# Kernel optimization log

Measured on AMD Instinct MI355X. Metric: run time of the kernel, lower is better.

## Reference

```python
import jax, jax.numpy as jnp
import numpy as np

STRIDE, PAD, DIL = 1, 1, 1
EPS = 1e-12
RHO_LIM = 1.0 - 1e-6
PI = jnp.pi


def clamp_pg(x, lo=0.0):
    # clamp value but pass gradient through (clamp_preserve_grad)
    return x + jax.lax.stop_gradient(jnp.maximum(x, lo) - x)


def setup_inputs() -> dict:
    key = jax.random.key(0)
    B, N, T, K = 8, 128, 1024, 3
    k = jax.random.uniform(key, (B, B, N, T, 2), dtype=jnp.float32)
    leak = jnp.array(1.0, dtype=jnp.float32)
    alpha = jnp.full((1, 1, K), 1.0 / K, dtype=jnp.float32)
    beta = jnp.array(0.0, dtype=jnp.float32)
    return {"k": k, "leak": leak, "alpha": alpha, "beta": beta}


def reference(k, leak, alpha, beta):
    k_gp, k_ntk = k[..., 0], k[..., 1]          # (B,B,N,T) each
    B, _, N, T = k_gp.shape

    # v[b,t] = k_gp[b,b,0,t]  (diagonal over batch dims, first lag)
    ar = jnp.arange(B)
    v = k_gp[ar, ar, 0, :]                      # (B,T)
    v_pad = jnp.pad(v, ((0, 0), (0, N - 1)))    # (B, T+N-1)

    v_xx = v[:, None, None, :]                  # (B,1,1,T)
    idx = jnp.arange(N)[:, None] + jnp.arange(T)[None, :]  # (N,T)
    v_yy = v_pad[:, idx][None]                  # (1,B,N,T): v_pad[b, n+t]

    # calculate_statistics
    std_x = jnp.sqrt(jnp.maximum(v_xx, 0.0))
    std_y = jnp.sqrt(jnp.maximum(v_yy, 0.0))
    denom = jnp.maximum(std_x * std_y, EPS)
    rho = jnp.clip(k_gp / denom, -RHO_LIM, RHO_LIM)  # (B,B,N,T)

    a = clamp_pg(leak)
    theta = jnp.arccos(rho)
    s = jnp.sqrt(1.0 - rho * rho)
    one_m = (1.0 - a) ** 2
    coef = 1.0 + a * a
    # leaky-ReLU arccos kernel and its derivative kernel
    c0 = std_x * std_y / (2.0 * PI) * (one_m * s + rho * (coef * PI - one_m * theta))
    c1 = (coef * PI - one_m * theta) / (2.0 * PI)

    w = clamp_pg(alpha)                         # (1,1,K)

    def conv(x):  # x: (B,B,N,T) -> (B,B,N,T')
        y = jax.lax.conv_general_dilated(
            x.reshape(-1, 1, T), w, window_strides=(STRIDE,),
            padding=[(PAD, PAD)], rhs_dilation=(DIL,),
            dimension_numbers=("NCH", "OIH", "NCH"))
        return y.reshape(B, B, N, -1)

    kg = conv(c0)
    kn = conv(c1 * k_ntk) + kg

    b = clamp_pg(beta)
    kg = kg + b
    kn = kn + b
    return jnp.stack([kg, kn], axis=-1)
```

## Files before the change

### kernel.cpp

```cpp
#include <hip/hip_runtime.h>
#include <math.h>

#define BDIM 8
#define NDIM 128
#define TDIM 1024
#define TPB 512

#define EPS_F 1e-12f
#define RHO_LIM_F (1.0f - 1e-6f)
#define PI_F 3.14159265358979323846f


__global__ __launch_bounds__(TPB) void conv_arccos_kernel(
    const float* __restrict__ k,
    const float* __restrict__ leak,
    const float* __restrict__ alpha,
    const float* __restrict__ beta,
    float* __restrict__ out)
{
    __shared__ float sc0[TDIM + 2];
    __shared__ float scn[TDIM + 2];

    const int row = blockIdx.x;
    const int n   = row % NDIM;
    const int bb  = row / NDIM;
    const int b2  = bb % BDIM;
    const int b1  = bb / BDIM;
    const int tid = threadIdx.x;
    const int t   = tid * 2;

    const float a   = fmaxf(leak[0], 0.0f);
    const float w0  = fmaxf(alpha[0], 0.0f);
    const float w1  = fmaxf(alpha[1], 0.0f);
    const float w2  = fmaxf(alpha[2], 0.0f);
    const float bia = fmaxf(beta[0], 0.0f);

    const float one_m  = (1.0f - a) * (1.0f - a);
    const float coef   = 1.0f + a * a;
    const float inv2pi = 0.15915494309189535f;

    const float4* krow4 = (const float4*)(k + (size_t)row * TDIM * 2);
    const float2* vrx = (const float2*)(k) + (size_t)(b1 * BDIM + b1) * NDIM * TDIM;
    const float2* vry = (const float2*)(k) + (size_t)(b2 * BDIM + b2) * NDIM * TDIM;

    if (tid == 0) { sc0[0] = 0.0f; scn[0] = 0.0f; sc0[TDIM + 1] = 0.0f; scn[TDIM + 1] = 0.0f; }

    const float4 kv  = krow4[tid];
    const float4 vx2 = ((const float4*)vrx)[tid];

    const int lim = TDIM - n;
    const float vy0 = (t     < lim) ? vry[n + t    ].x : 0.0f;
    const float vy1 = (t + 1 < lim) ? vry[n + t + 1].x : 0.0f;

    const float p0 = sqrtf(fmaxf(vx2.x, 0.0f) * fmaxf(vy0, 0.0f));
    const float p1 = sqrtf(fmaxf(vx2.z, 0.0f) * fmaxf(vy1, 0.0f));

    const float r0 = fminf(fmaxf(kv.x * __builtin_amdgcn_rcpf(fmaxf(p0, EPS_F)), -RHO_LIM_F), RHO_LIM_F);
    const float r1 = fminf(fmaxf(kv.z * __builtin_amdgcn_rcpf(fmaxf(p1, EPS_F)), -RHO_LIM_F), RHO_LIM_F);

    float c00, c01, cn0, cn1;
    if (one_m == 0.0f) {
        const float hc = 0.5f * coef;
        c00 = p0 * r0 * hc;
        c01 = p1 * r1 * hc;
        cn0 = hc * kv.y;
        cn1 = hc * kv.w;
    } else {
        const float th0 = acosf(r0), th1 = acosf(r1);
        const float s0 = sqrtf(1.0f - r0 * r0), s1 = sqrtf(1.0f - r1 * r1);
        const float br0 = coef * PI_F - one_m * th0;
        const float br1 = coef * PI_F - one_m * th1;
        c00 = p0 * inv2pi * (one_m * s0 + r0 * br0);
        c01 = p1 * inv2pi * (one_m * s1 + r1 * br1);
        cn0 = br0 * inv2pi * kv.y;
        cn1 = br1 * inv2pi * kv.w;
    }

    sc0[t + 1] = c00;
    sc0[t + 2] = c01;
    scn[t + 1] = cn0;
    scn[t + 2] = cn1;

    __syncthreads();

    const float c0l = sc0[t];
    const float c0r = sc0[t + 3];
    const float cnl = scn[t];
    const float cnr = scn[t + 3];

    const float kg0 = w0 * c0l + w1 * c00 + w2 * c01;
    const float kg1 = w0 * c00 + w1 * c01 + w2 * c0r;
    const float kn0 = w0 * cnl + w1 * cn0 + w2 * cn1 + kg0;
    const float kn1 = w0 * cn0 + w1 * cn1 + w2 * cnr + kg1;

    float4 o;
    o.x = kg0 + bia;
    o.y = kn0 + bia;
    o.z = kg1 + bia;
    o.w = kn1 + bia;
    ((float4*)(out + (size_t)row * TDIM * 2))[tid] = o;
}

extern "C" void kernel_launch(void* const* d_in, const int* in_sizes, int n_in,
                              void* d_out, int out_size, void* d_ws, size_t ws_size,
                              hipStream_t stream) {
    const float* k     = (const float*)d_in[0];
    const float* leak  = (const float*)d_in[1];
    const float* alpha = (const float*)d_in[2];
    const float* beta  = (const float*)d_in[3];
    float* out = (float*)d_out;

    const int n_rows = BDIM * BDIM * NDIM;
    conv_arccos_kernel<<<n_rows, TPB, 0, stream>>>(k, leak, alpha, beta, out);
}
```

Before: 126.1 us.

## Replace shared-memory halo exchange with wavefront shuffles and recompute edges

```diff
diff --git a/kernel.cpp b/kernel.cpp
--- a/kernel.cpp
+++ b/kernel.cpp
@@ -4,12 +4,32 @@
 #define BDIM 8
 #define NDIM 128
 #define TDIM 1024
-#define TPB 512
+#define TPB 256
 
 #define EPS_F 1e-12f
 #define RHO_LIM_F (1.0f - 1e-6f)
 #define PI_F 3.14159265358979323846f
 
+
+__device__ __forceinline__ void kfun(float kgp, float kntk, float vx, float vy,
+                                     float one_m, float coef, bool fast,
+                                     float& c0, float& cn)
+{
+    const float inv2pi = 0.15915494309189535f;
+    const float p = sqrtf(fmaxf(vx, 0.0f) * fmaxf(vy, 0.0f));
+    const float r = fminf(fmaxf(kgp * __builtin_amdgcn_rcpf(fmaxf(p, EPS_F)), -RHO_LIM_F), RHO_LIM_F);
+    if (fast) {
+        const float hc = 0.5f * coef;
+        c0 = p * r * hc;
+        cn = hc * kntk;
+    } else {
+        const float th = acosf(r);
+        const float s  = sqrtf(1.0f - r * r);
+        const float br = coef * PI_F - one_m * th;
+        c0 = p * inv2pi * (one_m * s + r * br);
+        cn = br * inv2pi * kntk;
+    }
+}
 
 __global__ __launch_bounds__(TPB) void conv_arccos_kernel(
     const float* __restrict__ k,
@@ -18,16 +38,13 @@
     const float* __restrict__ beta,
     float* __restrict__ out)
 {
-    __shared__ float sc0[TDIM + 2];
-    __shared__ float scn[TDIM + 2];
-
-    const int row = blockIdx.x;
-    const int n   = row % NDIM;
-    const int bb  = row / NDIM;
-    const int b2  = bb % BDIM;
-    const int b1  = bb / BDIM;
-    const int tid = threadIdx.x;
-    const int t   = tid * 2;
+    const int row  = blockIdx.x;
+    const int n    = row % NDIM;
+    const int bb   = row / NDIM;
+    const int b2   = bb % BDIM;
+    const int b1   = bb / BDIM;
+    const int tid  = threadIdx.x;
+    const int lane = tid & 63;
 
     const float a   = fmaxf(leak[0], 0.0f);
     const float w0  = fmaxf(alpha[0], 0.0f);
@@ -35,70 +52,64 @@
     const float w2  = fmaxf(alpha[2], 0.0f);
     const float bia = fmaxf(beta[0], 0.0f);
 
-    const float one_m  = (1.0f - a) * (1.0f - a);
-    const float coef   = 1.0f + a * a;
-    const float inv2pi = 0.15915494309189535f;
+    const float one_m = (1.0f - a) * (1.0f - a);
+    const float coef  = 1.0f + a * a;
+    const bool  fast  = (one_m == 0.0f);
 
     const float4* krow4 = (const float4*)(k + (size_t)row * TDIM * 2);
+    const float2* krow2 = (const float2*)(k + (size_t)row * TDIM * 2);
     const float2* vrx = (const float2*)(k) + (size_t)(b1 * BDIM + b1) * NDIM * TDIM;
     const float2* vry = (const float2*)(k) + (size_t)(b2 * BDIM + b2) * NDIM * TDIM;
-
-    if (tid == 0) { sc0[0] = 0.0f; scn[0] = 0.0f; sc0[TDIM + 1] = 0.0f; scn[TDIM + 1] = 0.0f; }
-
-    const float4 kv  = krow4[tid];
-    const float4 vx2 = ((const float4*)vrx)[tid];
+    float4* orow = (float4*)(out + (size_t)row * TDIM * 2);
 
     const int lim = TDIM - n;
-    const float vy0 = (t     < lim) ? vry[n + t    ].x : 0.0f;
-    const float vy1 = (t + 1 < lim) ? vry[n + t + 1].x : 0.0f;
 
-    const float p0 = sqrtf(fmaxf(vx2.x, 0.0f) * fmaxf(vy0, 0.0f));
-    const float p1 = sqrtf(fmaxf(vx2.z, 0.0f) * fmaxf(vy1, 0.0f));
+    #pragma unroll
+    for (int j = 0; j < TDIM / (2 * TPB); ++j) {
+        const int f = tid + j * TPB;
+        const int t = 2 * f;
 
-    const float r0 = fminf(fmaxf(kv.x * __builtin_amdgcn_rcpf(fmaxf(p0, EPS_F)), -RHO_LIM_F), RHO_LIM_F);
-    const float r1 = fminf(fmaxf(kv.z * __builtin_amdgcn_rcpf(fmaxf(p1, EPS_F)), -RHO_LIM_F), RHO_LIM_F);
+        const float4 kv  = krow4[f];
+        const float4 vx2 = ((const float4*)vrx)[f];
+        const float vy0 = (t     < lim) ? vry[n + t    ].x : 0.0f;
+        const float vy1 = (t + 1 < lim) ? vry[n + t + 1].x : 0.0f;
 
-    float c00, c01, cn0, cn1;
-    if (one_m == 0.0f) {
-        const float hc = 0.5f * coef;
-        c00 = p0 * r0 * hc;
-        c01 = p1 * r1 * hc;
-        cn0 = hc * kv.y;
-        cn1 = hc * kv.w;
-    } else {
-        const float th0 = acosf(r0), th1 = acosf(r1);
-        const float s0 = sqrtf(1.0f - r0 * r0), s1 = sqrtf(1.0f - r1 * r1);
-        const float br0 = coef * PI_F - one_m * th0;
-        const float br1 = coef * PI_F - one_m * th1;
-        c00 = p0 * inv2pi * (one_m * s0 + r0 * br0);
-        c01 = p1 * inv2pi * (one_m * s1 + r1 * br1);
-        cn0 = br0 * inv2pi * kv.y;
-        cn1 = br1 * inv2pi * kv.w;
+        float c00, cn0, c01, cn1;
+        kfun(kv.x, kv.y, vx2.x, vy0, one_m, coef, fast, c00, cn0);
+        kfun(kv.z, kv.w, vx2.z, vy1, one_m, coef, fast, c01, cn1);
+
+        float c0l = __shfl_up(c01, 1);
+        float cnl = __shfl_up(cn1, 1);
+        float c0r = __shfl_down(c00, 1);
+        float cnr = __shfl_down(cn0, 1);
+
+        const bool lo = (lane == 0);
+        const bool hi = (lane == 63);
+        if (lo || hi) {
+            const int e = lo ? (t - 1) : (t + 2);
+            float ec0 = 0.0f, ecn = 0.0f;
+            if (e >= 0 && e < TDIM) {
+                const float2 kp  = krow2[e];
+                const float  evx = vrx[e].x;
+                const float  evy = (e < lim) ? vry[n + e].x : 0.0f;
+                kfun(kp.x, kp.y, evx, evy, one_m, coef, fast, ec0, ecn);
+            }
+            if (lo) { c0l = ec0; cnl = ecn; }
+            else    { c0r = ec0; cnr = ecn; }
+        }
+
+        const float kg0 = w0 * c0l + w1 * c00 + w2 * c01;
+        const float kg1 = w0 * c00 + w1 * c01 + w2 * c0r;
+        const float kn0 = w0 * cnl + w1 * cn0 + w2 * cn1 + kg0;
+        const float kn1 = w0 * cn0 + w1 * cn1 + w2 * cnr + kg1;
+
+        float4 o;
+        o.x = kg0 + bia;
+        o.y = kn0 + bia;
+        o.z = kg1 + bia;
+        o.w = kn1 + bia;
+        orow[f] = o;
     }
-
-    sc0[t + 1] = c00;
-    sc0[t + 2] = c01;
-    scn[t + 1] = cn0;
-    scn[t + 2] = cn1;
-
-    __syncthreads();
-
-    const float c0l = sc0[t];
-    const float c0r = sc0[t + 3];
-    const float cnl = scn[t];
-    const float cnr = scn[t + 3];
-
-    const float kg0 = w0 * c0l + w1 * c00 + w2 * c01;
-    const float kg1 = w0 * c00 + w1 * c01 + w2 * c0r;
-    const float kn0 = w0 * cnl + w1 * cn0 + w2 * cn1 + kg0;
-    const float kn1 = w0 * cn0 + w1 * cn1 + w2 * cnr + kg1;
-
-    float4 o;
-    o.x = kg0 + bia;
-    o.y = kn0 + bia;
-    o.z = kg1 + bia;
-    o.w = kn1 + bia;
-    ((float4*)(out + (size_t)row * TDIM * 2))[tid] = o;
 }
 
 extern "C" void kernel_launch(void* const* d_in, const int* in_sizes, int n_in,
```

New measurement: 128.6 us. No clear change (+2.0%).
